# Kernel tuning notes

Measured on AMD Instinct MI355X. Metric: run time of the kernel, lower is better.

## Reference

```python
import jax, jax.numpy as jnp
import numpy as np

Q_HEADS, KV_HEADS, D_K, D_V = 16, 4, 128, 128
GROUPS = Q_HEADS // KV_HEADS


def setup_inputs() -> dict:
    key = jax.random.key(0)
    ks = jax.random.split(key, 7)
    b, s, d = 2, 2048, 2048
    scale = 1.0 / np.sqrt(d).astype(np.float32)
    return {
        "Q": jax.random.normal(ks[0], (b, s, d), jnp.float32),
        "K": jax.random.normal(ks[1], (b, s, d), jnp.float32),
        "V": jax.random.normal(ks[2], (b, s, d), jnp.float32),
        "Wq": jax.random.normal(ks[3], (d, D_K * Q_HEADS), jnp.float32) * scale,
        "Wk": jax.random.normal(ks[4], (d, D_K * KV_HEADS), jnp.float32) * scale,
        "Wv": jax.random.normal(ks[5], (d, D_V * KV_HEADS), jnp.float32) * scale,
        "Wo": jax.random.normal(ks[6], (D_V * KV_HEADS, d), jnp.float32) * scale,
    }


def reference(Q, K, V, Wq, Wk, Wv, Wo):
    b, lq, _ = Q.shape
    lk = K.shape[1]
    # projections -> (b, heads, len, d)
    q = (Q @ Wq).reshape(b, lq, Q_HEADS, D_K).transpose(0, 2, 1, 3)
    k = (K @ Wk).reshape(b, lk, KV_HEADS, D_K).transpose(0, 2, 1, 3)
    v = (V @ Wv).reshape(b, lk, KV_HEADS, D_V).transpose(0, 2, 1, 3)
    # GQA quirk: scores summed over group dim g before softmax
    qr = q.reshape(b, GROUPS, KV_HEADS, lq, D_K)
    scores = jnp.einsum('bghqd,bhkd->bhqk', qr, k) / jnp.asarray(D_K ** 0.5, q.dtype)
    causal = jnp.tril(jnp.ones((lq, lk), bool))
    scores = jnp.where(causal[None, None], scores, jnp.asarray(-1e9, scores.dtype))
    attn = jax.nn.softmax(scores, axis=-1)  # (b, kv_heads, lq, lk)
    out = jnp.einsum('bhqk,bhkd->bhqd', attn, v)  # (b, kv_heads, lq, d_v)
    out = out.transpose(0, 2, 1, 3).reshape(b, lq, KV_HEADS * D_V)
    return out @ Wo
```

## Files before the change

### kernel.cpp

```cpp
#include <hip/hip_runtime.h>
#include <hip/hip_bf16.h>

typedef __attribute__((ext_vector_type(8))) short short8;
typedef __attribute__((ext_vector_type(4))) float f32x4;

#define MFMA16 __builtin_amdgcn_mfma_f32_16x16x32_bf16

__device__ inline unsigned short f2bf(float f) {
  __hip_bfloat16 h = __float2bfloat16(f);
  unsigned short u;
  __builtin_memcpy(&u, &h, 2);
  return u;
}

__device__ inline float bf2f(unsigned short u) {
  unsigned int x = ((unsigned int)u) << 16;
  float f;
  __builtin_memcpy(&f, &x, 4);
  return f;
}

__device__ inline void storeC(unsigned short* p, float v) { *p = f2bf(v); }
__device__ inline void storeC(float* p, float v) { *p = v; }

__device__ inline void gload16(const void* g, void* l) {
  __builtin_amdgcn_global_load_lds(
      (const __attribute__((address_space(1))) unsigned int*)g,
      (__attribute__((address_space(3))) unsigned int*)l,
      16, 0, 0);
}

__global__ __launch_bounds__(256)
void wqsum_t(const float* __restrict__ wq, unsigned short* __restrict__ dst) {
  __shared__ float t[64][65];
  const int n0 = blockIdx.x * 64, d0 = blockIdx.y * 64;
  const int tid = threadIdx.x;
#pragma unroll
  for (int it = 0; it < 16; ++it) {
    const int idx = it * 256 + tid;
    const int dd = idx >> 6, nn = idx & 63;
    const float* p = wq + (size_t)(d0 + dd) * 2048 + n0 + nn;
    t[dd][nn] = p[0] + p[512] + p[1024] + p[1536];
  }
  __syncthreads();
#pragma unroll
  for (int it = 0; it < 16; ++it) {
    const int idx = it * 256 + tid;
    const int nn = idx >> 6, dd = idx & 63;
    dst[(size_t)(n0 + nn) * 2048 + d0 + dd] = f2bf(t[dd][nn]);
  }
}

__global__ __launch_bounds__(256)
void transpose_w(const float* __restrict__ src, unsigned short* __restrict__ dst,
                 int R, int C) {
  __shared__ float t[64][65];
  const int c0 = blockIdx.x * 64, r0 = blockIdx.y * 64;
  const int tid = threadIdx.x;
#pragma unroll
  for (int it = 0; it < 16; ++it) {
    const int idx = it * 256 + tid;
    const int r = idx >> 6, c = idx & 63;
    t[r][c] = src[(size_t)(r0 + r) * C + c0 + c];
  }
  __syncthreads();
#pragma unroll
  for (int it = 0; it < 16; ++it) {
    const int idx = it * 256 + tid;
    const int rr = idx >> 6, cc = idx & 63;
    dst[(size_t)(c0 + rr) * R + r0 + cc] = f2bf(t[cc][rr]);
  }
}

__global__ __launch_bounds__(256)
void vtrans(const unsigned short* __restrict__ vh, unsigned short* __restrict__ vt) {
  __shared__ unsigned short t[64][72];
  const int s0 = blockIdx.x * 64;
  const int d0 = blockIdx.y * 64;
  const int bh = blockIdx.z;
  const int brow = (bh >> 2) * 2048;
  const int h = bh & 3;
  const int tid = threadIdx.x;
#pragma unroll
  for (int it = 0; it < 2; ++it) {
    const int idx = it * 256 + tid;
    const int s = idx >> 3;
    const int dd = (idx & 7) << 3;
    *(short8*)&t[s][dd] =
        *(const short8*)(vh + (size_t)(brow + s0 + s) * 512 + h * 128 + d0 + dd);
  }
  __syncthreads();
#pragma unroll
  for (int it = 0; it < 2; ++it) {
    const int idx = it * 256 + tid;
    const int dd = idx >> 3;
    const int ss = (idx & 7) << 3;
    short8 o;
#pragma unroll
    for (int e = 0; e < 8; ++e) o[e] = (short)t[ss + e][dd];
    *(short8*)(vt + ((size_t)bh * 128 + d0 + dd) * 2048 + s0 + ss) = o;
  }
}

template <bool AF32, typename CT, int KS>
__global__ __launch_bounds__(256)
void gemm_bt(const void* A0, const void* A1, const void* A2,
             const unsigned short* __restrict__ Bt, CT* __restrict__ C,
             int K, int N, size_t sB, size_t sC) {
  __shared__ unsigned short As[128 * 64];
  __shared__ unsigned short Bs[128 * 64];

  const int tid = threadIdx.x;
  const int lane = tid & 63;
  const int wv = tid >> 6;
  const int wm = (wv >> 1) << 6;
  const int wn = (wv & 1) << 6;
  const int l15 = lane & 15;
  const int l4 = lane >> 4;
  const int lsw = (l15 & 7) << 4;

  const int nwg = gridDim.x;
  const int bid = blockIdx.x;
  const int job = (bid & 7) * (nwg >> 3) + (bid >> 3);
  const int ntile = N >> 7;
  const int per_ks = nwg / KS;
  const int ks = (KS > 1) ? (job / per_ks) : 0;
  const int jj = job - ks * per_ks;
  const int z = jj / (32 * ntile);
  const int rem = jj - z * 32 * ntile;
  const int m0 = (rem / ntile) << 7;
  const int n0 = (rem % ntile) << 7;
  const int kbeg = ks * (K / KS);
  const int kend = kbeg + K / KS;

  const void* Az = (z == 0) ? A0 : (z == 1) ? A1 : A2;
  const unsigned short* Ab = (const unsigned short*)Az;
  const float* Af = (const float*)Az;
  const unsigned short* Bz = Bt + sB * (size_t)z;

  const f32x4 zero = {0.f, 0.f, 0.f, 0.f};
  f32x4 acc[4][4];
#pragma unroll
  for (int i = 0; i < 4; ++i)
#pragma unroll
    for (int j = 0; j < 4; ++j) acc[i][j] = zero;

  const int srow = tid >> 3;
  const int scol = (tid & 7) << 3;
  const int scolsw = scol ^ ((srow & 7) << 3);

  float4 ar[8];

  auto issueB = [&](int k0) {
#pragma unroll
    for (int s = 0; s < 4; ++s) {
      const unsigned short* bsrc =
          Bz + (size_t)(n0 + srow + s * 32) * K + k0 + scolsw;
      gload16(bsrc, (char*)Bs + tid * 16 + s * 4096);
    }
  };
  auto issueA16 = [&](int k0) {
#pragma unroll
    for (int s = 0; s < 4; ++s) {
      const unsigned short* asrc =
          Ab + (size_t)(m0 + srow + s * 32) * K + k0 + scolsw;
      gload16(asrc, (char*)As + tid * 16 + s * 4096);
    }
  };
  auto loadA = [&](int k0) {
#pragma unroll
    for (int s = 0; s < 4; ++s) {
      const float* asrc = Af + (size_t)(m0 + srow + s * 32) * K + k0 + scol;
      ar[2 * s] = *(const float4*)(asrc);
      ar[2 * s + 1] = *(const float4*)(asrc + 4);
    }
  };
  auto writeA = [&]() {
#pragma unroll
    for (int s = 0; s < 4; ++s) {
      short8 o;
      o[0] = (short)f2bf(ar[2 * s].x); o[1] = (short)f2bf(ar[2 * s].y);
      o[2] = (short)f2bf(ar[2 * s].z); o[3] = (short)f2bf(ar[2 * s].w);
      o[4] = (short)f2bf(ar[2 * s + 1].x); o[5] = (short)f2bf(ar[2 * s + 1].y);
      o[6] = (short)f2bf(ar[2 * s + 1].z); o[7] = (short)f2bf(ar[2 * s + 1].w);
      *(short8*)((char*)As + (srow + s * 32) * 128 + scolsw * 2) = o;
    }
  };

  if constexpr (AF32) loadA(kbeg);

  for (int k0 = kbeg; k0 < kend; k0 += 64) {
    if constexpr (AF32) writeA(); else issueA16(k0);
    issueB(k0);
    if constexpr (AF32) {
      if (k0 + 64 < kend) loadA(k0 + 64);
    }
    __syncthreads();
#pragma unroll
    for (int kk = 0; kk < 2; ++kk) {
      const int kb = (kk * 64 + (l4 << 4)) ^ lsw;
      short8 a[4], b[4];
#pragma unroll
      for (int i = 0; i < 4; ++i)
        a[i] = *(const short8*)((const char*)As + (wm + i * 16 + l15) * 128 + kb);
#pragma unroll
      for (int j = 0; j < 4; ++j)
        b[j] = *(const short8*)((const char*)Bs + (wn + j * 16 + l15) * 128 + kb);
#pragma unroll
      for (int i = 0; i < 4; ++i)
#pragma unroll
        for (int j = 0; j < 4; ++j)
          acc[i][j] = MFMA16(a[i], b[j], acc[i][j], 0, 0, 0);
    }
    __syncthreads();
  }

  CT* Cz = C + sC * (size_t)(ks * 3 + z);
#pragma unroll
  for (int i = 0; i < 4; ++i) {
    const int row0 = m0 + wm + i * 16 + (l4 << 2);
#pragma unroll
    for (int j = 0; j < 4; ++j) {
      const int col = n0 + wn + j * 16 + l15;
#pragma unroll
      for (int r = 0; r < 4; ++r)
        storeC(&Cz[(size_t)(row0 + r) * N + col], acc[i][j][r]);
    }
  }
}

__global__ __launch_bounds__(256)
void qkv_combine(const unsigned short* __restrict__ pC,
                 unsigned short* __restrict__ dst) {
  const size_t HALF = 6291456;
  size_t i = ((size_t)blockIdx.x * 256 + threadIdx.x) * 8;
  const size_t stride = (size_t)gridDim.x * 256 * 8;
  for (; i < HALF; i += stride) {
    const short8 a = *(const short8*)(pC + i);
    const short8 b = *(const short8*)(pC + HALF + i);
    short8 o;
#pragma unroll
    for (int e = 0; e < 8; ++e)
      o[e] = (short)f2bf(bf2f((unsigned short)a[e]) + bf2f((unsigned short)b[e]));
    *(short8*)(dst + i) = o;
  }
}

__global__ __launch_bounds__(128)
void attn_split(const unsigned short* __restrict__ qh,
                const unsigned short* __restrict__ kh,
                const unsigned short* __restrict__ vt,
                unsigned short* __restrict__ Oh,
                unsigned short* __restrict__ pO,
                float* __restrict__ pml) {
  __shared__ unsigned short P_lds[2][32][36];
  const int tid = threadIdx.x;
  const int lane = tid & 63;
  const int wave = tid >> 6;
  const int l15 = lane & 15;
  const int l4 = lane >> 4;
  const int bh = blockIdx.x & 7;
  const int jid = blockIdx.x >> 3;
  const int brow = (bh >> 2) * 2048;
  const int h = bh & 3;

  int j = jid, g = 0;
  while (j >= 2 * (g + 1) * (g + 2)) ++g;
  const int rem = j - 2 * g * (g + 1);
  const int r_ = rem / (g + 1);
  const int c_ = rem - r_ * (g + 1);
  const int qt = 4 * g + r_;
  const int k_begin = c_ << 8;
  const int k_end = (c_ == g) ? (qt + 1) * 64 : ((c_ + 1) << 8);
  const int qrow_w = qt * 64 + wave * 32;
  const float SCALE2 = 0.127517424f;

  short8 qf[2][4];
#pragma unroll
  for (int m = 0; m < 2; ++m) {
    const unsigned short* qp =
        qh + (size_t)(brow + qrow_w + m * 16 + l15) * 512 + h * 128 + (l4 << 3);
#pragma unroll
    for (int kk = 0; kk < 4; ++kk) qf[m][kk] = *(const short8*)(qp + kk * 32);
  }

  short8 oneb;
#pragma unroll
  for (int e = 0; e < 8; ++e) oneb[e] = (short)0x3F80;

  const f32x4 zero = {0.f, 0.f, 0.f, 0.f};
  f32x4 o_acc[2][8];
  f32x4 l_acc[2];
#pragma unroll
  for (int m = 0; m < 2; ++m) {
    l_acc[m] = zero;
#pragma unroll
    for (int i = 0; i < 8; ++i) o_acc[m][i] = zero;
  }
  float m_run[2][4];
#pragma unroll
  for (int m = 0; m < 2; ++m)
#pragma unroll
    for (int r = 0; r < 4; ++r) m_run[m][r] = -1e30f;

  const int nt = (k_end - k_begin) >> 5;
  for (int t = 0; t < nt; ++t) {
    const int kbase = k_begin + t * 32;
    if (kbase > qrow_w + 31) continue;
    f32x4 sa[2][2];
    sa[0][0] = zero; sa[0][1] = zero; sa[1][0] = zero; sa[1][1] = zero;
#pragma unroll
    for (int n = 0; n < 2; ++n) {
      short8 kf[4];
      const unsigned short* kp =
          kh + (size_t)(brow + kbase + n * 16 + l15) * 512 + h * 128 + (l4 << 3);
#pragma unroll
      for (int kk = 0; kk < 4; ++kk) kf[kk] = *(const short8*)(kp + kk * 32);
#pragma unroll
      for (int kk = 0; kk < 4; ++kk) {
        sa[0][n] = MFMA16(qf[0][kk], kf[kk], sa[0][n], 0, 0, 0);
        sa[1][n] = MFMA16(qf[1][kk], kf[kk], sa[1][n], 0, 0, 0);
      }
    }
    const bool need_mask = (kbase + 31 > qrow_w);
    float p[2][2][4];
#pragma unroll
    for (int m = 0; m < 2; ++m)
#pragma unroll
      for (int n = 0; n < 2; ++n)
#pragma unroll
        for (int r = 0; r < 4; ++r) {
          float v = sa[m][n][r] * SCALE2;
          if (need_mask) {
            const int kc = kbase + n * 16 + l15;
            const int qr = qrow_w + m * 16 + (l4 << 2) + r;
            if (kc > qr) v = -1e30f;
          }
          p[m][n][r] = v;
        }
    float pmax[2][4];
#pragma unroll
    for (int m = 0; m < 2; ++m)
#pragma unroll
      for (int r = 0; r < 4; ++r) {
        float tmax = fmaxf(p[m][0][r], p[m][1][r]);
#pragma unroll
        for (int o = 1; o <= 8; o <<= 1) tmax = fmaxf(tmax, __shfl_xor(tmax, o));
        pmax[m][r] = tmax;
      }
#pragma unroll
    for (int m = 0; m < 2; ++m) {
      bool near = true;
#pragma unroll
      for (int r = 0; r < 4; ++r) near = near && (pmax[m][r] <= m_run[m][r] + 8.f);
      if (!__all(near)) {
#pragma unroll
        for (int r = 0; r < 4; ++r) {
          const float mn = fmaxf(m_run[m][r], pmax[m][r]);
          const float alpha = exp2f(m_run[m][r] - mn);
          m_run[m][r] = mn;
          l_acc[m][r] *= alpha;
#pragma unroll
          for (int d8 = 0; d8 < 8; ++d8) o_acc[m][d8][r] *= alpha;
        }
      }
    }
#pragma unroll
    for (int m = 0; m < 2; ++m)
#pragma unroll
      for (int n = 0; n < 2; ++n)
#pragma unroll
        for (int r = 0; r < 4; ++r)
          p[m][n][r] = exp2f(p[m][n][r] - m_run[m][r]);
#pragma unroll
    for (int m = 0; m < 2; ++m)
#pragma unroll
      for (int n = 0; n < 2; ++n)
#pragma unroll
        for (int r = 0; r < 4; ++r)
          P_lds[wave][m * 16 + (l4 << 2) + r][n * 16 + l15] = f2bf(p[m][n][r]);
    short8 pa[2];
#pragma unroll
    for (int m = 0; m < 2; ++m)
      pa[m] = *(const short8*)((const char*)&P_lds[wave][0][0] +
                               (m * 16 + l15) * 72 + (l4 << 4));
    l_acc[0] = MFMA16(pa[0], oneb, l_acc[0], 0, 0, 0);
    l_acc[1] = MFMA16(pa[1], oneb, l_acc[1], 0, 0, 0);
#pragma unroll
    for (int d8 = 0; d8 < 8; ++d8) {
      const short8 vb = *(const short8*)(
          vt + ((size_t)bh * 128 + d8 * 16 + l15) * 2048 + kbase + (l4 << 3));
      o_acc[0][d8] = MFMA16(pa[0], vb, o_acc[0][d8], 0, 0, 0);
      o_acc[1][d8] = MFMA16(pa[1], vb, o_acc[1][d8], 0, 0, 0);
    }
  }

  if (g == 0) {
#pragma unroll
    for (int m = 0; m < 2; ++m)
#pragma unroll
      for (int d8 = 0; d8 < 8; ++d8)
#pragma unroll
        for (int r = 0; r < 4; ++r) {
          const int row = brow + qrow_w + m * 16 + (l4 << 2) + r;
          Oh[(size_t)row * 512 + h * 128 + d8 * 16 + l15] =
              f2bf(o_acc[m][d8][r] / l_acc[m][r]);
        }
  } else {
    const int slot = bh * 144 + jid;
    unsigned short* po = pO + (size_t)slot * 64 * 128;
#pragma unroll
    for (int m = 0; m < 2; ++m)
#pragma unroll
      for (int d8 = 0; d8 < 8; ++d8)
#pragma unroll
        for (int r = 0; r < 4; ++r) {
          const int row = wave * 32 + m * 16 + (l4 << 2) + r;
          po[row * 128 + d8 * 16 + l15] = f2bf(o_acc[m][d8][r]);
        }
    if (l15 == 0) {
#pragma unroll
      for (int m = 0; m < 2; ++m)
#pragma unroll
        for (int r = 0; r < 4; ++r) {
          const int row = wave * 32 + m * 16 + (l4 << 2) + r;
          pml[((size_t)slot * 64 + row) * 2 + 0] = m_run[m][r];
          pml[((size_t)slot * 64 + row) * 2 + 1] = l_acc[m][r];
        }
    }
  }
}

__global__ __launch_bounds__(256)
void attn_combine(const unsigned short* __restrict__ pO,
                  const float* __restrict__ pml,
                  unsigned short* __restrict__ Oh) {
  const int bh = blockIdx.y;
  const int qt = 4 + blockIdx.x;
  const int g = qt >> 2;
  const int nch = g + 1;
  const int base = 2 * g * (g + 1) + (qt & 3) * (g + 1);
  const int slot0 = bh * 144 + base;
  const int brow = (bh >> 2) * 2048;
  const int h = bh & 3;
#pragma unroll
  for (int u = 0; u < 4; ++u) {
    const int unit = u * 256 + threadIdx.x;
    const int row = unit >> 4;
    const int c8 = (unit & 15) << 3;
    float M = -1e30f;
    for (int c = 0; c < nch; ++c)
      M = fmaxf(M, pml[((size_t)(slot0 + c) * 64 + row) * 2]);
    float L = 0.f;
    float acc[8] = {0.f, 0.f, 0.f, 0.f, 0.f, 0.f, 0.f, 0.f};
    for (int c = 0; c < nch; ++c) {
      const float mc = pml[((size_t)(slot0 + c) * 64 + row) * 2];
      const float lc = pml[((size_t)(slot0 + c) * 64 + row) * 2 + 1];
      const float w = exp2f(mc - M);
      L += w * lc;
      const short8 ov =
          *(const short8*)(pO + ((size_t)(slot0 + c) * 64 + row) * 128 + c8);
#pragma unroll
      for (int e = 0; e < 8; ++e) acc[e] += w * bf2f((unsigned short)ov[e]);
    }
    const float inv = 1.f / L;
    short8 o;
#pragma unroll
    for (int e = 0; e < 8; ++e) o[e] = (short)f2bf(acc[e] * inv);
    *(short8*)(Oh + (size_t)(brow + qt * 64 + row) * 512 + h * 128 + c8) = o;
  }
}

extern "C" void kernel_launch(void* const* d_in, const int* in_sizes, int n_in,
                              void* d_out, int out_size, void* d_ws, size_t ws_size,
                              hipStream_t stream) {
  const float* Q  = (const float*)d_in[0];
  const float* K_ = (const float*)d_in[1];
  const float* V  = (const float*)d_in[2];
  const float* Wq = (const float*)d_in[3];
  const float* Wk = (const float*)d_in[4];
  const float* Wv = (const float*)d_in[5];
  const float* Wo = (const float*)d_in[6];
  float* out = (float*)d_out;

  char* ws = (char*)d_ws;
  unsigned short* Wt  = (unsigned short*)ws;
  unsigned short* WoT = (unsigned short*)(ws + 6291456);
  unsigned short* qh  = (unsigned short*)(ws + 8388608);
  unsigned short* kh  = qh + 2097152;
  unsigned short* vh  = qh + 2 * 2097152;
  unsigned short* Oh  = qh + 3 * 2097152;
  unsigned short* vt  = (unsigned short*)(ws + 25165824);
  unsigned short* pO  = (unsigned short*)(ws + 29360128);
  float*          pml = (float*)(ws + 48234496);
  unsigned short* pC  = (unsigned short*)(ws + 20971520);

  wqsum_t<<<dim3(8, 32), 256, 0, stream>>>(Wq, Wt);
  transpose_w<<<dim3(8, 32), 256, 0, stream>>>(Wk, Wt + 1048576, 2048, 512);
  transpose_w<<<dim3(8, 32), 256, 0, stream>>>(Wv, Wt + 2097152, 2048, 512);
  transpose_w<<<dim3(32, 8), 256, 0, stream>>>(Wo, WoT, 512, 2048);

  gemm_bt<true, unsigned short, 2><<<768, 256, 0, stream>>>(
      Q, K_, V, Wt, pC, 2048, 512, 1048576, 2097152);
  qkv_combine<<<1024, 256, 0, stream>>>(pC, qh);

  vtrans<<<dim3(32, 2, 8), 256, 0, stream>>>(vh, vt);

  attn_split<<<1152, 128, 0, stream>>>(qh, kh, vt, Oh, pO, pml);
  attn_combine<<<dim3(28, 8), 256, 0, stream>>>(pO, pml, Oh);

  gemm_bt<false, float, 1><<<512, 256, 0, stream>>>(
      Oh, Oh, Oh, WoT, out, 512, 2048, 0, 0);
}
```

Before: 155.3 us.

## Double-buffer GEMM B tiles and fold V split-K combine into vtrans

```diff
diff --git a/kernel.cpp b/kernel.cpp
--- a/kernel.cpp
+++ b/kernel.cpp
@@ -73,7 +73,7 @@
 }
 
 __global__ __launch_bounds__(256)
-void vtrans(const unsigned short* __restrict__ vh, unsigned short* __restrict__ vt) {
+void vtrans(const unsigned short* __restrict__ pC, unsigned short* __restrict__ vt) {
   __shared__ unsigned short t[64][72];
   const int s0 = blockIdx.x * 64;
   const int d0 = blockIdx.y * 64;
@@ -81,13 +81,21 @@
   const int brow = (bh >> 2) * 2048;
   const int h = bh & 3;
   const int tid = threadIdx.x;
+  const unsigned short* va = pC + 4194304;
+  const unsigned short* vb = pC + 6291456 + 4194304;
 #pragma unroll
   for (int it = 0; it < 2; ++it) {
     const int idx = it * 256 + tid;
     const int s = idx >> 3;
     const int dd = (idx & 7) << 3;
-    *(short8*)&t[s][dd] =
-        *(const short8*)(vh + (size_t)(brow + s0 + s) * 512 + h * 128 + d0 + dd);
+    const size_t off = (size_t)(brow + s0 + s) * 512 + h * 128 + d0 + dd;
+    const short8 xa = *(const short8*)(va + off);
+    const short8 xb = *(const short8*)(vb + off);
+    short8 o;
+#pragma unroll
+    for (int e = 0; e < 8; ++e)
+      o[e] = (short)f2bf(bf2f((unsigned short)xa[e]) + bf2f((unsigned short)xb[e]));
+    *(short8*)&t[s][dd] = o;
   }
   __syncthreads();
 #pragma unroll
@@ -107,8 +115,8 @@
 void gemm_bt(const void* A0, const void* A1, const void* A2,
              const unsigned short* __restrict__ Bt, CT* __restrict__ C,
              int K, int N, size_t sB, size_t sC) {
-  __shared__ unsigned short As[128 * 64];
-  __shared__ unsigned short Bs[128 * 64];
+  __shared__ unsigned short As[AF32 ? 1 : 2][128 * 64];
+  __shared__ unsigned short Bs[2][128 * 64];
 
   const int tid = threadIdx.x;
   const int lane = tid & 63;
@@ -151,20 +159,20 @@
 
   float4 ar[8];
 
-  auto issueB = [&](int k0) {
+  auto issueB = [&](int buf, int k0) {
 #pragma unroll
     for (int s = 0; s < 4; ++s) {
       const unsigned short* bsrc =
           Bz + (size_t)(n0 + srow + s * 32) * K + k0 + scolsw;
-      gload16(bsrc, (char*)Bs + tid * 16 + s * 4096);
+      gload16(bsrc, (char*)&Bs[buf][0] + tid * 16 + s * 4096);
     }
   };
-  auto issueA16 = [&](int k0) {
+  auto issueA16 = [&](int buf, int k0) {
 #pragma unroll
     for (int s = 0; s < 4; ++s) {
       const unsigned short* asrc =
           Ab + (size_t)(m0 + srow + s * 32) * K + k0 + scolsw;
-      gload16(asrc, (char*)As + tid * 16 + s * 4096);
+      gload16(asrc, (char*)&As[buf][0] + tid * 16 + s * 4096);
     }
   };
   auto loadA = [&](int k0) {
@@ -183,36 +191,45 @@
       o[2] = (short)f2bf(ar[2 * s].z); o[3] = (short)f2bf(ar[2 * s].w);
       o[4] = (short)f2bf(ar[2 * s + 1].x); o[5] = (short)f2bf(ar[2 * s + 1].y);
       o[6] = (short)f2bf(ar[2 * s + 1].z); o[7] = (short)f2bf(ar[2 * s + 1].w);
-      *(short8*)((char*)As + (srow + s * 32) * 128 + scolsw * 2) = o;
+      *(short8*)((char*)&As[0][0] + (srow + s * 32) * 128 + scolsw * 2) = o;
     }
   };
 
-  if constexpr (AF32) loadA(kbeg);
-
+  if constexpr (AF32) loadA(kbeg); else issueA16(0, kbeg);
+  issueB(0, kbeg);
+
+  int cur = 0;
   for (int k0 = kbeg; k0 < kend; k0 += 64) {
-    if constexpr (AF32) writeA(); else issueA16(k0);
-    issueB(k0);
+    const bool more = (k0 + 64 < kend);
+    asm volatile("s_waitcnt vmcnt(0)" ::: "memory");
     if constexpr (AF32) {
-      if (k0 + 64 < kend) loadA(k0 + 64);
-    }
-    __syncthreads();
+      writeA();
+      if (more) { issueB(cur ^ 1, k0 + 64); loadA(k0 + 64); }
+      asm volatile("s_waitcnt lgkmcnt(0)" ::: "memory");
+    } else {
+      if (more) { issueA16(cur ^ 1, k0 + 64); issueB(cur ^ 1, k0 + 64); }
+    }
+    __builtin_amdgcn_s_barrier();
+    const unsigned short* as = AF32 ? &As[0][0] : &As[cur][0];
 #pragma unroll
     for (int kk = 0; kk < 2; ++kk) {
       const int kb = (kk * 64 + (l4 << 4)) ^ lsw;
       short8 a[4], b[4];
 #pragma unroll
       for (int i = 0; i < 4; ++i)
-        a[i] = *(const short8*)((const char*)As + (wm + i * 16 + l15) * 128 + kb);
+        a[i] = *(const short8*)((const char*)as + (wm + i * 16 + l15) * 128 + kb);
 #pragma unroll
       for (int j = 0; j < 4; ++j)
-        b[j] = *(const short8*)((const char*)Bs + (wn + j * 16 + l15) * 128 + kb);
+        b[j] = *(const short8*)((const char*)&Bs[cur][0] +
+                                (wn + j * 16 + l15) * 128 + kb);
 #pragma unroll
       for (int i = 0; i < 4; ++i)
 #pragma unroll
         for (int j = 0; j < 4; ++j)
           acc[i][j] = MFMA16(a[i], b[j], acc[i][j], 0, 0, 0);
     }
-    __syncthreads();
+    __builtin_amdgcn_s_barrier();
+    cur ^= 1;
   }
 
   CT* Cz = C + sC * (size_t)(ks * 3 + z);
@@ -232,12 +249,13 @@
 __global__ __launch_bounds__(256)
 void qkv_combine(const unsigned short* __restrict__ pC,
                  unsigned short* __restrict__ dst) {
-  const size_t HALF = 6291456;
+  const size_t COUNT = 4194304;
+  const size_t OFF = 6291456;
   size_t i = ((size_t)blockIdx.x * 256 + threadIdx.x) * 8;
   const size_t stride = (size_t)gridDim.x * 256 * 8;
-  for (; i < HALF; i += stride) {
+  for (; i < COUNT; i += stride) {
     const short8 a = *(const short8*)(pC + i);
-    const short8 b = *(const short8*)(pC + HALF + i);
+    const short8 b = *(const short8*)(pC + OFF + i);
     short8 o;
 #pragma unroll
     for (int e = 0; e < 8; ++e)
@@ -488,7 +506,6 @@
   unsigned short* WoT = (unsigned short*)(ws + 6291456);
   unsigned short* qh  = (unsigned short*)(ws + 8388608);
   unsigned short* kh  = qh + 2097152;
-  unsigned short* vh  = qh + 2 * 2097152;
   unsigned short* Oh  = qh + 3 * 2097152;
   unsigned short* vt  = (unsigned short*)(ws + 25165824);
   unsigned short* pO  = (unsigned short*)(ws + 29360128);
@@ -503,8 +520,7 @@
   gemm_bt<true, unsigned short, 2><<<768, 256, 0, stream>>>(
       Q, K_, V, Wt, pC, 2048, 512, 1048576, 2097152);
   qkv_combine<<<1024, 256, 0, stream>>>(pC, qh);
-
-  vtrans<<<dim3(32, 2, 8), 256, 0, stream>>>(vh, vt);
+  vtrans<<<dim3(32, 2, 8), 256, 0, stream>>>(pC, vt);
 
   attn_split<<<1152, 128, 0, stream>>>(qh, kh, vt, Oh, pO, pml);
   attn_combine<<<dim3(28, 8), 256, 0, stream>>>(pO, pml, Oh);
```

After: 151.6 us. 2.4% less time.
